# Optimization experiments

Measured on AMD Instinct MI355X. Metric: run time of the kernel, lower is better.

Reference implementation:

```python
import jax, jax.numpy as jnp
import numpy as np

B, DIM, H_IN, H_OUT = 256, 16, 32, 32
IN_F, OUT_F = DIM * H_IN, DIM * H_OUT  # 512, 512


def _masks():
    rb = jnp.arange(OUT_F) // H_OUT  # row block id
    cb = jnp.arange(IN_F) // H_IN    # col block id
    mask_d = (rb[:, None] == cb[None, :]).astype(jnp.float32)  # block diagonal
    mask_o = (rb[:, None] > cb[None, :]).astype(jnp.float32)   # strictly lower block triangular
    return mask_d, mask_o


def setup_inputs() -> dict:
    key = jax.random.key(0)
    k1, k2, k3, k4, k5 = jax.random.split(key, 5)
    return {
        "inputs": jax.random.normal(k1, (B, IN_F), dtype=jnp.float32),
        "hyper_w": jax.random.normal(k2, (B, OUT_F, IN_F), dtype=jnp.float32),
        "hyper_b": jax.random.normal(k3, (B, OUT_F), dtype=jnp.float32),
        "log_grad_cumul": jax.random.normal(k4, (B, DIM, H_IN, 1), dtype=jnp.float32),
        "scale_factor": jax.random.uniform(k5, (1,), dtype=jnp.float32),
    }


def reference(inputs, hyper_w, hyper_b, log_grad_cumul, scale_factor):
    mask_d, mask_o = _masks()
    # per-sample weight build: exp on diagonal blocks, identity on lower blocks
    w = jnp.exp(hyper_w) * mask_d + hyper_w * mask_o  # [B, OUT, IN]
    # scaled Frobenius norm per sample
    w_F2 = jnp.sum(w * w, axis=(-2, -1), keepdims=True)  # [B,1,1]
    w_normed = jnp.exp(scale_factor) * w / jnp.sqrt(w_F2)
    # diagonal-block entries of hyper_w -> [B, DIM, H_OUT, H_IN]
    hw4 = hyper_w.reshape(B, DIM, H_OUT, DIM, H_IN)
    diag = jnp.moveaxis(jnp.diagonal(hw4, axis1=1, axis2=3), -1, 1)
    log_grad_dh = scale_factor + diag - 0.5 * jnp.log(w_F2)[..., None]
    # batched matvec + bias
    outputs = jnp.einsum('boi,bi->bo', w_normed, inputs) + hyper_b
    # logsumexp jacobian accumulation
    lg = log_grad_dh[..., None, :] + jnp.swapaxes(log_grad_cumul, -2, -1)[:, :, None, :, :]
    out_log_det = jax.scipy.special.logsumexp(lg, axis=-1)  # [B, DIM, H_OUT, 1]
    return outputs, out_log_det
```

## Files before the change

kernel.cpp:

```cpp
#include <hip/hip_runtime.h>
#include <math.h>


#define OUT_OFF 131072

__global__ __launch_bounds__(256) void mw_main(
    const float* __restrict__ hw,
    const float* __restrict__ x,
    const float* __restrict__ lgc,
    float* __restrict__ out,
    float* __restrict__ f2_partial)
{
    const int blk = blockIdx.x;
    const int b  = blk >> 4;
    const int rb = blk & 15;
    const int t  = threadIdx.x;
    const int r   = t >> 3;
    const int sub = t & 7;
    const int o = rb * 32 + r;

    const float4* __restrict__ row4 = (const float4*)(hw + ((size_t)(b * 512 + o)) * 512);
    const float4* __restrict__ x4   = (const float4*)(x + (size_t)b * 512);

    float acc = 0.0f;
    float f2  = 0.0f;

    #pragma unroll 2
    for (int j = 0; j < rb; ++j) {
        float4 v  = row4[j * 8 + sub];
        float4 xv = x4[j * 8 + sub];
        acc += v.x * xv.x + v.y * xv.y + v.z * xv.z + v.w * xv.w;
        f2  += v.x * v.x + v.y * v.y + v.z * v.z + v.w * v.w;
    }

    float m, s;
    {
        float4 v  = row4[rb * 8 + sub];
        float4 xv = x4[rb * 8 + sub];
        float4 l4 = ((const float4*)(lgc + (size_t)b * 512 + rb * 32))[sub];
        float e0 = expf(v.x), e1 = expf(v.y), e2 = expf(v.z), e3 = expf(v.w);
        acc += e0 * xv.x + e1 * xv.y + e2 * xv.z + e3 * xv.w;
        f2  += e0 * e0 + e1 * e1 + e2 * e2 + e3 * e3;
        float a0 = v.x + l4.x, a1 = v.y + l4.y, a2 = v.z + l4.z, a3 = v.w + l4.w;
        m = fmaxf(fmaxf(a0, a1), fmaxf(a2, a3));
        s = expf(a0 - m) + expf(a1 - m) + expf(a2 - m) + expf(a3 - m);
    }

    #pragma unroll
    for (int d = 1; d < 8; d <<= 1) {
        acc += __shfl_xor(acc, d, 64);
        float mo = __shfl_xor(m, d, 64);
        float so = __shfl_xor(s, d, 64);
        float mn = fmaxf(m, mo);
        s = s * expf(m - mn) + so * expf(mo - mn);
        m = mn;
    }
    if (sub == 0) {
        out[b * 512 + o]           = acc;
        out[OUT_OFF + b * 512 + o] = m + logf(s);
    }

    #pragma unroll
    for (int d = 1; d < 64; d <<= 1) f2 += __shfl_xor(f2, d, 64);
    __shared__ float sf[4];
    if ((t & 63) == 0) sf[t >> 6] = f2;
    __syncthreads();
    if (t == 0) f2_partial[b * 16 + rb] = sf[0] + sf[1] + sf[2] + sf[3];
}

__global__ __launch_bounds__(256) void mw_final(
    const float* __restrict__ f2_partial,
    const float* __restrict__ hb,
    const float* __restrict__ scale,
    float* __restrict__ out)
{
    const int b = blockIdx.x;
    const int t = threadIdx.x;

    float f2 = 0.0f;
    #pragma unroll
    for (int k = 0; k < 16; ++k) f2 += f2_partial[b * 16 + k];

    const float sc     = scale[0];
    const float coef   = expf(sc) / sqrtf(f2);
    const float logoff = sc - 0.5f * logf(f2);

    #pragma unroll
    for (int k = 0; k < 2; ++k) {
        const int o  = t + k * 256;
        const int io = b * 512 + o;
        out[io]           = coef * out[io] + hb[io];
        out[OUT_OFF + io] += logoff;
    }
}

extern "C" void kernel_launch(void* const* d_in, const int* in_sizes, int n_in,
                              void* d_out, int out_size, void* d_ws, size_t ws_size,
                              hipStream_t stream) {
    const float* x     = (const float*)d_in[0];
    const float* hw    = (const float*)d_in[1];
    const float* hb    = (const float*)d_in[2];
    const float* lgc   = (const float*)d_in[3];
    const float* scale = (const float*)d_in[4];
    float* out = (float*)d_out;
    float* f2p = (float*)d_ws;

    mw_main<<<dim3(256 * 16), dim3(256), 0, stream>>>(hw, x, lgc, out, f2p);
    mw_final<<<dim3(256), dim3(256), 0, stream>>>(f2p, hb, scale, out);
}
```

Before: 344.2 us.

## Pair triangular row blocks per workgroup to balance load, stage x in LDS

Each workgroup now handles row block pr together with row block 15-pr, so every block reads the same total number of lower-triangular column blocks instead of anywhere from 1 to 16. The input vector and the log-grad slices are staged once in shared memory. Weight loads use nontemporal hints because the hyper-weight stream is read only once. The grid is halved and the partial norm array shrinks to 8 entries per sample, which cuts per-workgroup parallelism in exchange for even work per block.

```diff
diff --git a/kernel.cpp b/kernel.cpp
--- a/kernel.cpp
+++ b/kernel.cpp
@@ -3,6 +3,8 @@
 
 
 #define OUT_OFF 131072
+
+typedef float f4 __attribute__((ext_vector_type(4)));
 
 __global__ __launch_bounds__(256) void mw_main(
     const float* __restrict__ hw,
@@ -12,60 +14,92 @@
     float* __restrict__ f2_partial)
 {
     const int blk = blockIdx.x;
-    const int b  = blk >> 4;
-    const int rb = blk & 15;
-    const int t  = threadIdx.x;
+    const int b   = blk >> 3;
+    const int pr  = blk & 7;
+    const int rbA = pr;
+    const int rbB = 15 - pr;
+    const int t   = threadIdx.x;
     const int r   = t >> 3;
     const int sub = t & 7;
-    const int o = rb * 32 + r;
 
-    const float4* __restrict__ row4 = (const float4*)(hw + ((size_t)(b * 512 + o)) * 512);
-    const float4* __restrict__ x4   = (const float4*)(x + (size_t)b * 512);
+    __shared__ f4 xs[128];
+    __shared__ f4 ls[16];
+    if (t < 128) xs[t] = ((const f4*)(x + (size_t)b * 512))[t];
+    if (t >= 128 && t < 136) ls[t - 128] = ((const f4*)(lgc + (size_t)b * 512 + rbA * 32))[t - 128];
+    if (t >= 136 && t < 144) ls[t - 128] = ((const f4*)(lgc + (size_t)b * 512 + rbB * 32))[t - 136];
+    __syncthreads();
 
-    float acc = 0.0f;
-    float f2  = 0.0f;
+    const f4* __restrict__ rowA = (const f4*)(hw + ((size_t)(b * 512 + rbA * 32 + r)) * 512);
+    const f4* __restrict__ rowB = (const f4*)(hw + ((size_t)(b * 512 + rbB * 32 + r)) * 512);
 
+    float accA = 0.f, f2A = 0.f, accB = 0.f, f2B = 0.f;
+
+    int j = 0;
     #pragma unroll 2
-    for (int j = 0; j < rb; ++j) {
-        float4 v  = row4[j * 8 + sub];
-        float4 xv = x4[j * 8 + sub];
-        acc += v.x * xv.x + v.y * xv.y + v.z * xv.z + v.w * xv.w;
-        f2  += v.x * v.x + v.y * v.y + v.z * v.z + v.w * v.w;
+    for (; j < rbA; ++j) {
+        f4 va = __builtin_nontemporal_load(rowA + j * 8 + sub);
+        f4 vb = __builtin_nontemporal_load(rowB + j * 8 + sub);
+        f4 xv = xs[j * 8 + sub];
+        accA += va.x * xv.x + va.y * xv.y + va.z * xv.z + va.w * xv.w;
+        f2A  += va.x * va.x + va.y * va.y + va.z * va.z + va.w * va.w;
+        accB += vb.x * xv.x + vb.y * xv.y + vb.z * xv.z + vb.w * xv.w;
+        f2B  += vb.x * vb.x + vb.y * vb.y + vb.z * vb.z + vb.w * vb.w;
+    }
+    #pragma unroll 4
+    for (; j < rbB; ++j) {
+        f4 vb = __builtin_nontemporal_load(rowB + j * 8 + sub);
+        f4 xv = xs[j * 8 + sub];
+        accB += vb.x * xv.x + vb.y * xv.y + vb.z * xv.z + vb.w * xv.w;
+        f2B  += vb.x * vb.x + vb.y * vb.y + vb.z * vb.z + vb.w * vb.w;
     }
 
-    float m, s;
+    float mA, sA, mB, sB;
     {
-        float4 v  = row4[rb * 8 + sub];
-        float4 xv = x4[rb * 8 + sub];
-        float4 l4 = ((const float4*)(lgc + (size_t)b * 512 + rb * 32))[sub];
-        float e0 = expf(v.x), e1 = expf(v.y), e2 = expf(v.z), e3 = expf(v.w);
-        acc += e0 * xv.x + e1 * xv.y + e2 * xv.z + e3 * xv.w;
-        f2  += e0 * e0 + e1 * e1 + e2 * e2 + e3 * e3;
-        float a0 = v.x + l4.x, a1 = v.y + l4.y, a2 = v.z + l4.z, a3 = v.w + l4.w;
-        m = fmaxf(fmaxf(a0, a1), fmaxf(a2, a3));
-        s = expf(a0 - m) + expf(a1 - m) + expf(a2 - m) + expf(a3 - m);
+        f4 va = __builtin_nontemporal_load(rowA + rbA * 8 + sub);
+        f4 vb = __builtin_nontemporal_load(rowB + rbB * 8 + sub);
+        f4 xa = xs[rbA * 8 + sub];
+        f4 xb = xs[rbB * 8 + sub];
+        f4 la = ls[sub];
+        f4 lb = ls[8 + sub];
+        float e0 = expf(va.x), e1 = expf(va.y), e2 = expf(va.z), e3 = expf(va.w);
+        accA += e0 * xa.x + e1 * xa.y + e2 * xa.z + e3 * xa.w;
+        f2A  += e0 * e0 + e1 * e1 + e2 * e2 + e3 * e3;
+        float a0 = va.x + la.x, a1 = va.y + la.y, a2 = va.z + la.z, a3 = va.w + la.w;
+        mA = fmaxf(fmaxf(a0, a1), fmaxf(a2, a3));
+        sA = expf(a0 - mA) + expf(a1 - mA) + expf(a2 - mA) + expf(a3 - mA);
+        float g0 = expf(vb.x), g1 = expf(vb.y), g2 = expf(vb.z), g3 = expf(vb.w);
+        accB += g0 * xb.x + g1 * xb.y + g2 * xb.z + g3 * xb.w;
+        f2B  += g0 * g0 + g1 * g1 + g2 * g2 + g3 * g3;
+        float b0 = vb.x + lb.x, b1 = vb.y + lb.y, b2 = vb.z + lb.z, b3 = vb.w + lb.w;
+        mB = fmaxf(fmaxf(b0, b1), fmaxf(b2, b3));
+        sB = expf(b0 - mB) + expf(b1 - mB) + expf(b2 - mB) + expf(b3 - mB);
     }
 
     #pragma unroll
     for (int d = 1; d < 8; d <<= 1) {
-        acc += __shfl_xor(acc, d, 64);
-        float mo = __shfl_xor(m, d, 64);
-        float so = __shfl_xor(s, d, 64);
-        float mn = fmaxf(m, mo);
-        s = s * expf(m - mn) + so * expf(mo - mn);
-        m = mn;
+        accA += __shfl_xor(accA, d, 64);
+        accB += __shfl_xor(accB, d, 64);
+        float mo, so, mn;
+        mo = __shfl_xor(mA, d, 64); so = __shfl_xor(sA, d, 64);
+        mn = fmaxf(mA, mo); sA = sA * expf(mA - mn) + so * expf(mo - mn); mA = mn;
+        mo = __shfl_xor(mB, d, 64); so = __shfl_xor(sB, d, 64);
+        mn = fmaxf(mB, mo); sB = sB * expf(mB - mn) + so * expf(mo - mn); mB = mn;
     }
     if (sub == 0) {
-        out[b * 512 + o]           = acc;
-        out[OUT_OFF + b * 512 + o] = m + logf(s);
+        const int oA = rbA * 32 + r, oB = rbB * 32 + r;
+        out[b * 512 + oA]           = accA;
+        out[OUT_OFF + b * 512 + oA] = mA + logf(sA);
+        out[b * 512 + oB]           = accB;
+        out[OUT_OFF + b * 512 + oB] = mB + logf(sB);
     }
 
+    float f2 = f2A + f2B;
     #pragma unroll
     for (int d = 1; d < 64; d <<= 1) f2 += __shfl_xor(f2, d, 64);
     __shared__ float sf[4];
     if ((t & 63) == 0) sf[t >> 6] = f2;
     __syncthreads();
-    if (t == 0) f2_partial[b * 16 + rb] = sf[0] + sf[1] + sf[2] + sf[3];
+    if (t == 0) f2_partial[b * 8 + pr] = sf[0] + sf[1] + sf[2] + sf[3];
 }
 
 __global__ __launch_bounds__(256) void mw_final(
@@ -79,7 +113,7 @@
 
     float f2 = 0.0f;
     #pragma unroll
-    for (int k = 0; k < 16; ++k) f2 += f2_partial[b * 16 + k];
+    for (int k = 0; k < 8; ++k) f2 += f2_partial[b * 8 + k];
 
     const float sc     = scale[0];
     const float coef   = expf(sc) / sqrtf(f2);
@@ -105,6 +139,6 @@
     float* out = (float*)d_out;
     float* f2p = (float*)d_ws;
 
-    mw_main<<<dim3(256 * 16), dim3(256), 0, stream>>>(hw, x, lgc, out, f2p);
+    mw_main<<<dim3(256 * 8), dim3(256), 0, stream>>>(hw, x, lgc, out, f2p);
     mw_final<<<dim3(256), dim3(256), 0, stream>>>(f2p, hb, scale, out);
 }
```

Measured after the change: 326.6 us. 5.1% less time.
